# Optimization experiments

Hardware: AMD Instinct MI355X
Metric: run time of the kernel (lower is better)

The kernel has to match this reference:

```python
import jax, jax.numpy as jnp
import numpy as np

DIM = 64

def conv2d_g2(x, w, b):
    # 3x3 conv, padding=1, groups=2, NCHW
    y = jax.lax.conv_general_dilated(x, w, (1, 1), [(1, 1), (1, 1)],
                                     dimension_numbers=('NCHW', 'OIHW', 'NCHW'),
                                     feature_group_count=2)
    return y + b[None, :, None, None]

def bilinear_gather(x, py, px):
    # x: [B,C,H,W]; py,px: [B,K,H,W] float sample coords -> [B,K,H,W,C]
    B, C, H, W = x.shape
    y0 = jnp.floor(py); x0 = jnp.floor(px)
    ly = py - y0; lx = px - x0
    hy = 1.0 - ly; hx = 1.0 - lx
    b_idx = jnp.arange(B)[:, None, None, None]
    def gather(yi, xi):
        valid = (yi >= 0) & (yi < H) & (xi >= 0) & (xi < W)
        yc = jnp.clip(yi, 0, H - 1).astype(jnp.int32)
        xc = jnp.clip(xi, 0, W - 1).astype(jnp.int32)
        v = x[b_idx, :, yc, xc]  # [B,K,H,W,C]
        return v * valid[..., None].astype(x.dtype)
    return (gather(y0, x0) * (hy * hx)[..., None]
            + gather(y0, x0 + 1) * (hy * lx)[..., None]
            + gather(y0 + 1, x0) * (ly * hx)[..., None]
            + gather(y0 + 1, x0 + 1) * (ly * lx)[..., None])

def deform_dw(x, offset, w, b, k, pad, dil):
    # depthwise (groups=C, offset_groups=1) deformable conv, stride 1
    B, C, H, W = x.shape
    K = k * k
    off = offset.reshape(B, K, 2, H, W)  # torchvision layout: (dy,dx) per kernel tap
    ky = jnp.repeat(jnp.arange(k), k).astype(x.dtype)   # [K]
    kx = jnp.tile(jnp.arange(k), k).astype(x.dtype)     # [K]
    base_y = jnp.arange(H, dtype=x.dtype)[None, None, :, None] - pad + dil * ky[None, :, None, None]
    base_x = jnp.arange(W, dtype=x.dtype)[None, None, None, :] - pad + dil * kx[None, :, None, None]
    py = base_y + off[:, :, 0]  # [B,K,H,W]
    px = base_x + off[:, :, 1]
    val = bilinear_gather(x, py, px)  # [B,K,H,W,C]
    return jnp.einsum('bkhwc,ck->bchw', val, w.reshape(C, K)) + b[None, :, None, None]

def lsk_forward(x, w_off3, b_off3, w_off2, b_off2, w7, b7, w5, b5):
    B, C, H, W = x.shape
    offset3 = conv2d_g2(x, w_off3, b_off3)            # [B,98,H,W]
    out1 = deform_dw(x, offset3, w7, b7, 7, 9, 3)     # [B,C,H,W]
    offset2 = conv2d_g2(x, w_off2, b_off2)            # [B,50,H,W]
    out2 = deform_dw(out1, offset2, w5, b5, 5, 6, 3)  # [B,C,H,W]
    feats = jnp.stack([out1, out2], axis=1)           # [B,2,C,H,W]
    gap = feats.mean(axis=(3, 4), keepdims=True)      # [B,2,C,1,1]
    attn = jax.nn.softmax(gap, axis=1)
    return jnp.sum(feats * attn, axis=1)              # [B,C,H,W]

def setup_inputs() -> dict:
    key = jax.random.key(0)
    ks = jax.random.split(key, 9)
    B, C, H, W = 4, DIM, 56, 56
    return {
        'x':      jax.random.normal(ks[0], (B, C, H, W), jnp.float32),
        'w_off3': jax.random.normal(ks[1], (98, C // 2, 3, 3), jnp.float32) * 0.05,
        'b_off3': jax.random.normal(ks[2], (98,), jnp.float32) * 0.05,
        'w_off2': jax.random.normal(ks[3], (50, C // 2, 3, 3), jnp.float32) * 0.05,
        'b_off2': jax.random.normal(ks[4], (50,), jnp.float32) * 0.05,
        'w7':     jax.random.normal(ks[5], (C, 1, 7, 7), jnp.float32) * 0.1,
        'b7':     jax.random.normal(ks[6], (C,), jnp.float32) * 0.05,
        'w5':     jax.random.normal(ks[7], (C, 1, 5, 5), jnp.float32) * 0.1,
        'b5':     jax.random.normal(ks[8], (C,), jnp.float32) * 0.05,
    }

def reference(x, w_off3, b_off3, w_off2, b_off2, w7, b7, w5, b5):
    return lsk_forward(x, w_off3, b_off3, w_off2, b_off2, w7, b7, w5, b5)
```

## Files before the change

kernel.cpp:

```cpp
#include <hip/hip_runtime.h>
#include <hip/hip_fp16.h>
#include <math.h>

#define HH 56
#define WW 56
#define CC 64
#define BB 4
#define HWA (HH*WW)

typedef _Float16 half8_t __attribute__((ext_vector_type(8)));
typedef _Float16 h2_t   __attribute__((ext_vector_type(2)));
typedef float f32x4_t __attribute__((ext_vector_type(4)));

#define PROWS 57
#define PSTRB (PROWS*57*64*4)
#define ROWSTRB (57*64*4)

__global__ __launch_bounds__(256)
void k_prep(const float* __restrict__ x,
            const float* __restrict__ w3, const float* __restrict__ w2,
            const float* __restrict__ b3, const float* __restrict__ b2,
            __half2* __restrict__ xp, _Float16* __restrict__ xh,
            _Float16* __restrict__ Wp, float* __restrict__ bbp) {
    int blk = blockIdx.x;
    int tid = threadIdx.x;
    if (blk < BB*56) {
        __shared__ float ld[64*57];
        int b = blk / 56, y = blk % 56;
        for (int i = tid; i < 64*56; i += 256) {
            int c = i / 56, col = i % 56;
            ld[c*57 + col] = x[((size_t)b*CC + c)*HWA + y*WW + col];
        }
        __syncthreads();
        for (int i = tid; i < 57*64; i += 256) {
            int j = i >> 6, c = i & 63;
            float lo = (j > 0)  ? ld[c*57 + j - 1] : 0.f;
            float hi = (j < 56) ? ld[c*57 + j]     : 0.f;
            xp[((size_t)(b*PROWS + y)*57 + j)*CC + c] = __floats2half2_rn(lo, hi);
        }
        _Float16* dst = xh + (((size_t)(b*2)*56 + y)*58)*32;
        for (int i = tid; i < 2*58*32; i += 256) {
            int g = i / 1856;
            int r = i % 1856;
            int col = r / 32, ic = r % 32;
            float v = 0.f;
            if (col >= 1 && col <= 56) v = ld[(g*32 + ic)*57 + col - 1];
            dst[(size_t)g*56*58*32 + r] = (_Float16)v;
        }
    } else {
        int i = (blk - BB*56)*256 + tid;
        if (i < 46080) {
            int j    = i & 7;
            int lane = (i >> 3) & 63;
            int mt   = (i >> 9) % 5;
            int kt   = (i / 2560) % 9;
            int g    = i / 23040;
            int m  = mt*16 + (lane & 15);
            int ic = (lane >> 4)*8 + j;
            int ky = kt/3, kx = kt%3;
            float v = 0.f;
            if (m < 49)      v = w3[((g*49 + m)*32 + ic)*9 + ky*3 + kx];
            else if (m < 74) v = w2[((g*25 + (m-49))*32 + ic)*9 + ky*3 + kx];
            Wp[i] = (_Float16)v;
        } else if (i < 46240) {
            int t = i - 46080; int g = t/80, m = t%80;
            float v = 0.f;
            if (m < 49)      v = b3[g*49 + m];
            else if (m < 74) v = b2[g*25 + (m-49)];
            bbp[t] = v;
        }
    }
}

__global__ __launch_bounds__(256)
void k_convmfma(const _Float16* __restrict__ xh, const _Float16* __restrict__ Wp,
                const float* __restrict__ bb,
                float* __restrict__ off3, float* __restrict__ off2) {
    __shared__ _Float16 tile[4][3*18*32];
    int blk = blockIdx.x;
    int iy = blk % 56;
    int g  = (blk / 56) & 1;
    int b  = blk / 112;
    int wv   = threadIdx.y;
    int lane = threadIdx.x;
    int n0 = wv * 16;

    const unsigned int* xs = (const unsigned int*)xh;
    unsigned int* tl = (unsigned int*)&tile[wv][0];
#pragma unroll
    for (int i = 0; i < 14; ++i) {
        int idx = i*64 + lane;
        if (idx < 864) {
            int ic2 = idx & 15;
            int seg = idx >> 4;
            int cl = seg % 18, r = seg / 18;
            int y = iy - 1 + r, col = n0 + cl;
            unsigned int v = 0;
            if (y >= 0 && y < 56 && col < 58)
                v = xs[(((size_t)(b*2+g)*56 + y)*58 + col)*16 + ic2];
            tl[idx] = v;
        }
    }
    __syncthreads();

    int nlo = lane & 15, khi = lane >> 4;
    f32x4_t acc[5];
#pragma unroll
    for (int mt = 0; mt < 5; ++mt) acc[mt] = (f32x4_t){0.f,0.f,0.f,0.f};

    const half8_t* wp8 = (const half8_t*)Wp;
#pragma unroll
    for (int kt = 0; kt < 9; ++kt) {
        int ky = kt/3, kx = kt%3;
        half8_t bfrag = *(const half8_t*)&tile[wv][((ky*18) + nlo + kx)*32 + khi*8];
#pragma unroll
        for (int mt = 0; mt < 5; ++mt) {
            half8_t afrag = wp8[(((size_t)g*9 + kt)*5 + mt)*64 + lane];
            acc[mt] = __builtin_amdgcn_mfma_f32_16x16x32_f16(afrag, bfrag, acc[mt], 0, 0, 0);
        }
    }

    int pixcol = n0 + nlo;
    if (pixcol < 56) {
        int pix = iy*WW + pixcol;
#pragma unroll
        for (int mt = 0; mt < 5; ++mt) {
#pragma unroll
            for (int r = 0; r < 4; ++r) {
                int m = mt*16 + khi*4 + r;
                if (m < 74) {
                    float val = acc[mt][r] + bb[g*80 + m];
                    if (m < 49)
                        off3[((size_t)b*98 + g*49 + m)*HWA + pix] = val;
                    else
                        off2[((size_t)b*50 + g*25 + (m-49))*HWA + pix] = val;
                }
            }
        }
    }
}

template<int K, int KS, int PAD, bool WP>
__global__ __launch_bounds__(256)
void k_deform(const _Float16* __restrict__ xp, const float* __restrict__ off,
              const float* __restrict__ wg, const float* __restrict__ bias,
              float* __restrict__ out, float* __restrict__ partial,
              _Float16* __restrict__ xpo) {
    __shared__ float lw[K*65];
    __shared__ float loffs[2*K][16];
    __shared__ int4  lmeta[16][K];
    __shared__ float red[16][64];
    int tid = threadIdx.x + threadIdx.y*64;
    int blk = blockIdx.x;
    int xcd = blk & 7;
    int idx = blk >> 3;
    int b   = xcd >> 1;
    int hw0 = (xcd & 1)*(HWA/2) + idx*16;

    for (int i = tid; i < K*64; i += 256) {
        int c = i / K, t = i % K;
        lw[t*65 + c] = wg[i];
    }
    for (int i = tid; i < 8*K; i += 256) {
        int row = i >> 2, q4 = i & 3;
        float4 v = *(const float4*)&off[((size_t)b*2*K + row)*HWA + hw0 + q4*4];
        loffs[row][q4*4 + 0] = v.x; loffs[row][q4*4 + 1] = v.y;
        loffs[row][q4*4 + 2] = v.z; loffs[row][q4*4 + 3] = v.w;
    }
    __syncthreads();
    for (int i = tid; i < 16*K; i += 256) {
        int p = i / K, t = i % K;
        int hw = hw0 + p;
        int h = hw / WW, w = hw % WW;
        int ky = t / KS, kx = t % KS;
        float py = (float)(h - PAD + 3*ky) + loffs[2*t][p];
        float px = (float)(w - PAD + 3*kx) + loffs[2*t+1][p];
        float y0f = floorf(py), x0f = floorf(px);
        float ly = py - y0f, lx = px - x0f;
        float hy = 1.f - ly, hx = 1.f - lx;
        int y0 = (int)y0f, x0 = (int)x0f;
        int j = x0 + 1;
        bool jv = (j >= 0) && (j <= 56);
        int jc = jv ? j : 0;
        float s0 = ((y0   >= 0) && (y0   < HH) && jv) ? hy : 0.f;
        float s1 = ((y0+1 >= 0) && (y0+1 < HH) && jv) ? ly : 0.f;
        bool use1 = (s0 == 0.f);
        int rbase = use1 ? min(max(y0 + 1, 0), 55) : y0;
        float aw = use1 ? s1 : s0;
        float bw = use1 ? 0.f : s1;
        int4 m;
        m.x = (rbase*57 + jc)*(64*4);
        m.y = 0;
        __half2 wa = __floats2half2_rn(aw*hx, aw*lx);
        __half2 wb = __floats2half2_rn(bw*hx, bw*lx);
        m.z = *(int*)&wa;
        m.w = *(int*)&wb;
        lmeta[p][t] = m;
    }
    __syncthreads();

    int yp = threadIdx.y;
    int c  = threadIdx.x;
    const char* xc = (const char*)xp + (size_t)b*PSTRB + c*4;

    float acc[4] = {0.f, 0.f, 0.f, 0.f};
#pragma unroll 2
    for (int t = 0; t < K; ++t) {
        float lwv = lw[t*65 + c];
#pragma unroll
        for (int s = 0; s < 4; ++s) {
            int4 m = lmeta[yp + 4*s][t];
            h2_t r0 = *(const h2_t*)(xc + m.x);
            h2_t r1 = *(const h2_t*)(xc + m.x + ROWSTRB);
            float v = __builtin_amdgcn_fdot2(r0, *(h2_t*)&m.z, 0.f, false);
            v = __builtin_amdgcn_fdot2(r1, *(h2_t*)&m.w, v, false);
            acc[s] = fmaf(v, lwv, acc[s]);
        }
    }
    float bs = bias[c];
#pragma unroll
    for (int s = 0; s < 4; ++s) {
        float val = acc[s] + bs;
        int hw = hw0 + yp + 4*s;
        out[((size_t)b*HWA + hw)*CC + c] = val;
        if (WP) {
            int y = hw / WW, w = hw % WW;
            _Float16* base = xpo + ((size_t)(b*PROWS + y)*57)*CC*2;
            _Float16 hv = (_Float16)val;
            base[((w    )*64 + c)*2 + 1] = hv;
            base[((w + 1)*64 + c)*2 + 0] = hv;
            if (w == 0)  base[(c)*2 + 0] = (_Float16)0.f;
            if (w == 55) base[((56)*64 + c)*2 + 1] = (_Float16)0.f;
        }
        red[yp + 4*s][c] = val;
    }
    __syncthreads();
    if (yp == 0) {
        float s = 0.f;
#pragma unroll
        for (int r = 0; r < 16; ++r) s += red[r][c];
        partial[((size_t)b*(HWA/16) + (hw0 >> 4))*64 + c] = s;
    }
}

__global__ void k_gapA(const float* __restrict__ p1, const float* __restrict__ p2,
                       float* __restrict__ g2) {
    __shared__ float red[4][64];
    int blk = blockIdx.x;
    int chunk = blk % 7;
    int bf    = blk / 7;
    int b     = bf >> 1;
    const float* p = (bf & 1) ? p2 : p1;
    int tid = threadIdx.x;
    int c = tid & 63, s = tid >> 6;
    float sum = 0.f;
#pragma unroll
    for (int i = 0; i < 7; ++i) {
        int j = chunk*28 + s + 4*i;
        sum += p[((size_t)b*(HWA/16) + j)*64 + c];
    }
    red[s][c] = sum;
    __syncthreads();
    if (s == 0)
        g2[((size_t)bf*7 + chunk)*64 + c]
            = red[0][c] + red[1][c] + red[2][c] + red[3][c];
}

__global__ void k_combine(const float* __restrict__ o1, const float* __restrict__ o2,
                          const float* __restrict__ g2, float* __restrict__ out) {
    __shared__ float tile[64][65];
    __shared__ float gsh[2][64];
    int blk = blockIdx.x;
    int b   = blk / (HWA/64);
    int t0  = (blk % (HWA/64)) * 64;
    int tid = threadIdx.x;
    int c = tid & 63, q = tid >> 6;

    if (tid < 128) {
        int f = tid >> 6, cc = tid & 63;
        float s = 0.f;
#pragma unroll
        for (int k = 0; k < 7; ++k)
            s += g2[((size_t)(b*2+f)*7 + k)*64 + cc];
        gsh[f][cc] = s * (1.f/HWA);
    }
    __syncthreads();

    float g1v = gsh[0][c];
    float g2v = gsh[1][c];
    float m  = fmaxf(g1v, g2v);
    float e1 = expf(g1v - m), e2 = expf(g2v - m);
    float a1 = e1 / (e1 + e2), a2 = 1.f - a1;

#pragma unroll
    for (int i = 0; i < 16; ++i) {
        int p = q + 4*i;
        size_t idx = ((size_t)b*HWA + t0 + p)*CC + c;
        tile[p][c] = o1[idx]*a1 + o2[idx]*a2;
    }
    __syncthreads();
    int p2 = tid & 63;
#pragma unroll
    for (int i = 0; i < 16; ++i) {
        int c2 = q + 4*i;
        out[((size_t)b*CC + c2)*HWA + t0 + p2] = tile[p2][c2];
    }
}

extern "C" void kernel_launch(void* const* d_in, const int* in_sizes, int n_in,
                              void* d_out, int out_size, void* d_ws, size_t ws_size,
                              hipStream_t stream) {
    const float* x      = (const float*)d_in[0];
    const float* w_off3 = (const float*)d_in[1];
    const float* b_off3 = (const float*)d_in[2];
    const float* w_off2 = (const float*)d_in[3];
    const float* b_off2 = (const float*)d_in[4];
    const float* w7     = (const float*)d_in[5];
    const float* b7     = (const float*)d_in[6];
    const float* w5     = (const float*)d_in[7];
    const float* b5     = (const float*)d_in[8];
    float* out = (float*)d_out;

    const size_t PAIRF = (size_t)BB*PROWS*57*64;
    float* ws    = (float*)d_ws;
    float* off3r = ws;
    float* off2r = off3r + 1229312;
    float* out1  = off2r + 627200;
    float* out2  = out1  + 802816;
    float* xp1f  = out2  + 802816;
    float* xp2f  = xp1f  + PAIRF;
    float* xhf   = xp2f  + PAIRF;
    float* part1 = xhf   + 415744;
    float* part2 = part1 + 50176;
    float* gpA   = part2 + 50176;
    float* wpf   = gpA   + 3584;
    float* bbp   = wpf   + 23040;
    __half2*  xp1 = (__half2*)xp1f;
    _Float16* xp2h = (_Float16*)xp2f;
    _Float16* xh  = (_Float16*)xhf;
    _Float16* Wp  = (_Float16*)wpf;
    size_t need = (size_t)(1229312 + 627200 + 802816*2 + 831744*2 + 415744
                           + 50176*2 + 3584 + 23040 + 160) * 4;
    if (ws_size < need) return;

    k_prep<<<BB*56 + 181, 256, 0, stream>>>(x, w_off3, w_off2, b_off3, b_off2,
                                            xp1, xh, Wp, bbp);
    k_convmfma<<<BB*2*56, dim3(64,4), 0, stream>>>(xh, Wp, bbp, off3r, off2r);
    k_deform<49,7,9,true><<<BB*(HWA/16), dim3(64,4), 0, stream>>>(
        (const _Float16*)xp1, off3r, w7, b7, out1, part1, xp2h);
    k_deform<25,5,6,false><<<BB*(HWA/16), dim3(64,4), 0, stream>>>(
        xp2h, off2r, w5, b5, out2, part2, nullptr);
    k_gapA<<<8*7, 256, 0, stream>>>(part1, part2, gpA);
    k_combine<<<BB*(HWA/64), 256, 0, stream>>>(out1, out2, gpA, out);
}
```

Before: 149.8 us.

## Drop fp32 deform outputs, reuse fp16 padded copy, fold GAP reduction into combine

The first deformable stage no longer writes a separate fp32 output. The combine kernel reads out1 from the fp16 padded buffer that already feeds the second stage. The second stage writes its output in fp16 instead of fp32. The separate GAP partial-reduction kernel is removed, and each combine block now sums all 196 partials per channel itself. This cuts global write/read traffic and one launch, but it adds fp16 rounding to the final outputs and has every combine block redo a serial 196-step reduction.

Result: no change. 151.7 us (+1.3%).

```diff
diff --git a/kernel.cpp b/kernel.cpp
--- a/kernel.cpp
+++ b/kernel.cpp
@@ -144,7 +144,7 @@
 __global__ __launch_bounds__(256)
 void k_deform(const _Float16* __restrict__ xp, const float* __restrict__ off,
               const float* __restrict__ wg, const float* __restrict__ bias,
-              float* __restrict__ out, float* __restrict__ partial,
+              _Float16* __restrict__ outh, float* __restrict__ partial,
               _Float16* __restrict__ xpo) {
     __shared__ float lw[K*65];
     __shared__ float loffs[2*K][16];
@@ -222,7 +222,6 @@
     for (int s = 0; s < 4; ++s) {
         float val = acc[s] + bs;
         int hw = hw0 + yp + 4*s;
-        out[((size_t)b*HWA + hw)*CC + c] = val;
         if (WP) {
             int y = hw / WW, w = hw % WW;
             _Float16* base = xpo + ((size_t)(b*PROWS + y)*57)*CC*2;
@@ -231,6 +230,8 @@
             base[((w + 1)*64 + c)*2 + 0] = hv;
             if (w == 0)  base[(c)*2 + 0] = (_Float16)0.f;
             if (w == 55) base[((56)*64 + c)*2 + 1] = (_Float16)0.f;
+        } else {
+            outh[((size_t)b*HWA + hw)*CC + c] = (_Float16)val;
         }
         red[yp + 4*s][c] = val;
     }
@@ -243,31 +244,9 @@
     }
 }
 
-__global__ void k_gapA(const float* __restrict__ p1, const float* __restrict__ p2,
-                       float* __restrict__ g2) {
-    __shared__ float red[4][64];
-    int blk = blockIdx.x;
-    int chunk = blk % 7;
-    int bf    = blk / 7;
-    int b     = bf >> 1;
-    const float* p = (bf & 1) ? p2 : p1;
-    int tid = threadIdx.x;
-    int c = tid & 63, s = tid >> 6;
-    float sum = 0.f;
-#pragma unroll
-    for (int i = 0; i < 7; ++i) {
-        int j = chunk*28 + s + 4*i;
-        sum += p[((size_t)b*(HWA/16) + j)*64 + c];
-    }
-    red[s][c] = sum;
-    __syncthreads();
-    if (s == 0)
-        g2[((size_t)bf*7 + chunk)*64 + c]
-            = red[0][c] + red[1][c] + red[2][c] + red[3][c];
-}
-
-__global__ void k_combine(const float* __restrict__ o1, const float* __restrict__ o2,
-                          const float* __restrict__ g2, float* __restrict__ out) {
+__global__ void k_combine(const _Float16* __restrict__ xp2, const _Float16* __restrict__ o2h,
+                          const float* __restrict__ p1, const float* __restrict__ p2,
+                          float* __restrict__ out) {
     __shared__ float tile[64][65];
     __shared__ float gsh[2][64];
     int blk = blockIdx.x;
@@ -278,10 +257,10 @@
 
     if (tid < 128) {
         int f = tid >> 6, cc = tid & 63;
+        const float* p = f ? p2 : p1;
         float s = 0.f;
-#pragma unroll
-        for (int k = 0; k < 7; ++k)
-            s += g2[((size_t)(b*2+f)*7 + k)*64 + cc];
+        for (int j = 0; j < HWA/16; ++j)
+            s += p[((size_t)b*(HWA/16) + j)*64 + cc];
         gsh[f][cc] = s * (1.f/HWA);
     }
     __syncthreads();
@@ -295,15 +274,18 @@
 #pragma unroll
     for (int i = 0; i < 16; ++i) {
         int p = q + 4*i;
-        size_t idx = ((size_t)b*HWA + t0 + p)*CC + c;
-        tile[p][c] = o1[idx]*a1 + o2[idx]*a2;
-    }
-    __syncthreads();
-    int p2 = tid & 63;
+        int hw = t0 + p;
+        int y = hw / WW, w = hw % WW;
+        _Float16 h1 = xp2[(((size_t)(b*PROWS + y)*57 + w)*CC + c)*2 + 1];
+        _Float16 h2v = o2h[((size_t)b*HWA + hw)*CC + c];
+        tile[p][c] = (float)h1*a1 + (float)h2v*a2;
+    }
+    __syncthreads();
+    int p2i = tid & 63;
 #pragma unroll
     for (int i = 0; i < 16; ++i) {
         int c2 = q + 4*i;
-        out[((size_t)b*CC + c2)*HWA + t0 + p2] = tile[p2][c2];
+        out[((size_t)b*CC + c2)*HWA + t0 + p2i] = tile[p2i][c2];
     }
 }
 
@@ -325,31 +307,29 @@
     float* ws    = (float*)d_ws;
     float* off3r = ws;
     float* off2r = off3r + 1229312;
-    float* out1  = off2r + 627200;
-    float* out2  = out1  + 802816;
-    float* xp1f  = out2  + 802816;
+    float* xp1f  = off2r + 627200;
     float* xp2f  = xp1f  + PAIRF;
     float* xhf   = xp2f  + PAIRF;
-    float* part1 = xhf   + 415744;
+    float* o2hf  = xhf   + 415744;
+    float* part1 = o2hf  + 401408;
     float* part2 = part1 + 50176;
-    float* gpA   = part2 + 50176;
-    float* wpf   = gpA   + 3584;
+    float* wpf   = part2 + 50176;
     float* bbp   = wpf   + 23040;
     __half2*  xp1 = (__half2*)xp1f;
     _Float16* xp2h = (_Float16*)xp2f;
     _Float16* xh  = (_Float16*)xhf;
+    _Float16* o2h = (_Float16*)o2hf;
     _Float16* Wp  = (_Float16*)wpf;
-    size_t need = (size_t)(1229312 + 627200 + 802816*2 + 831744*2 + 415744
-                           + 50176*2 + 3584 + 23040 + 160) * 4;
+    size_t need = (size_t)(1229312 + 627200 + 831744*2 + 415744 + 401408
+                           + 50176*2 + 23040 + 160) * 4;
     if (ws_size < need) return;
 
     k_prep<<<BB*56 + 181, 256, 0, stream>>>(x, w_off3, w_off2, b_off3, b_off2,
                                             xp1, xh, Wp, bbp);
     k_convmfma<<<BB*2*56, dim3(64,4), 0, stream>>>(xh, Wp, bbp, off3r, off2r);
     k_deform<49,7,9,true><<<BB*(HWA/16), dim3(64,4), 0, stream>>>(
-        (const _Float16*)xp1, off3r, w7, b7, out1, part1, xp2h);
+        (const _Float16*)xp1, off3r, w7, b7, nullptr, part1, xp2h);
     k_deform<25,5,6,false><<<BB*(HWA/16), dim3(64,4), 0, stream>>>(
-        xp2h, off2r, w5, b5, out2, part2, nullptr);
-    k_gapA<<<8*7, 256, 0, stream>>>(part1, part2, gpA);
-    k_combine<<<BB*(HWA/64), 256, 0, stream>>>(out1, out2, gpA, out);
-}
+        xp2h, off2r, w5, b5, o2h, part2, nullptr);
+    k_combine<<<BB*(HWA/64), 256, 0, stream>>>(xp2h, o2h, part1, part2, out);
+}
```
